# Kernel optimization log

Hardware: AMD Instinct MI355X
Metric: run time of the kernel (lower is better)

## Reference

```python
import jax, jax.numpy as jnp
import numpy as np

DIM = 512
HEADS = 4
HEAD_DIM = DIM // HEADS
HIDDEN = DIM * 2
DEPTH = 4
N = 32768
T = 4  # fixed branch/token dim


def _layernorm(x, w, b, eps=1e-5):
    m = jnp.mean(x, axis=-1, keepdims=True)
    v = jnp.mean(jnp.square(x - m), axis=-1, keepdims=True)
    return (x - m) * jax.lax.rsqrt(v + eps) * w + b


def setup_inputs() -> dict:
    key = jax.random.key(0)
    ks = jax.random.split(key, 24)
    s = 0.02
    d = {
        'x': jax.random.normal(ks[0], (N, DIM, T), dtype=jnp.float32),
        'branch_embed': s * jax.random.normal(ks[1], (T, DIM), dtype=jnp.float32),
        'ln1_w': jnp.ones((DEPTH, DIM), jnp.float32),
        'ln1_b': jnp.zeros((DEPTH, DIM), jnp.float32),
        'qkv_w': s * jax.random.normal(ks[2], (DEPTH, 3 * DIM, DIM), dtype=jnp.float32),
        'qkv_b': jnp.zeros((DEPTH, 3 * DIM), jnp.float32),
        'proj_w': s * jax.random.normal(ks[3], (DEPTH, DIM, DIM), dtype=jnp.float32),
        'proj_b': jnp.zeros((DEPTH, DIM), jnp.float32),
        'ln2_w': jnp.ones((DEPTH, DIM), jnp.float32),
        'ln2_b': jnp.zeros((DEPTH, DIM), jnp.float32),
        'ffn_w1': s * jax.random.normal(ks[4], (DEPTH, HIDDEN, DIM), dtype=jnp.float32),
        'ffn_b1': jnp.zeros((DEPTH, HIDDEN), jnp.float32),
        'ffn_w2': s * jax.random.normal(ks[5], (DEPTH, DIM, HIDDEN), dtype=jnp.float32),
        'ffn_b2': jnp.zeros((DEPTH, DIM), jnp.float32),
        'pool_q': s * jax.random.normal(ks[6], (DIM,), dtype=jnp.float32),
        'pool_w': s * jax.random.normal(ks[7], (DIM, DIM), dtype=jnp.float32),
        'out_ln_w': jnp.ones((DIM,), jnp.float32),
        'out_ln_b': jnp.zeros((DIM,), jnp.float32),
        'out_w1': s * jax.random.normal(ks[8], (DIM // 2, DIM), dtype=jnp.float32),
        'out_b1': jnp.zeros((DIM // 2,), jnp.float32),
        'out_w2': s * jax.random.normal(ks[9], (1, DIM // 2), dtype=jnp.float32),
        'out_b2': jnp.zeros((1,), jnp.float32),
    }
    return d


def reference(x, branch_embed, ln1_w, ln1_b, qkv_w, qkv_b, proj_w, proj_b,
              ln2_w, ln2_b, ffn_w1, ffn_b1, ffn_w2, ffn_b2,
              pool_q, pool_w, out_ln_w, out_ln_b, out_w1, out_b1, out_w2, out_b2):
    # (N, C, 4) -> (N, 4, C), add branch embedding
    x = jnp.swapaxes(x, 1, 2) + branch_embed[None]
    n = x.shape[0]
    scale = 1.0 / np.sqrt(HEAD_DIM)
    for i in range(DEPTH):
        # --- MHSA (pre-LN, eval mode -> dropout off) ---
        h = _layernorm(x, ln1_w[i], ln1_b[i])
        qkv = jnp.einsum('ntd,ed->nte', h, qkv_w[i]) + qkv_b[i]  # (N, T, 3D)
        q, k, v = jnp.split(qkv, 3, axis=-1)
        q = q.reshape(n, T, HEADS, HEAD_DIM).transpose(0, 2, 1, 3)
        k = k.reshape(n, T, HEADS, HEAD_DIM).transpose(0, 2, 1, 3)
        v = v.reshape(n, T, HEADS, HEAD_DIM).transpose(0, 2, 1, 3)
        scores = jnp.einsum('nhqd,nhkd->nhqk', q, k) * scale
        attn = jax.nn.softmax(scores, axis=-1)
        o = jnp.einsum('nhqk,nhkd->nhqd', attn, v)
        o = o.transpose(0, 2, 1, 3).reshape(n, T, DIM)
        o = jnp.einsum('ntd,ed->nte', o, proj_w[i]) + proj_b[i]
        x = x + o
        # --- FFN ---
        h = _layernorm(x, ln2_w[i], ln2_b[i])
        f = jax.nn.gelu(jnp.einsum('ntd,hd->nth', h, ffn_w1[i]) + ffn_b1[i], approximate=False)
        f = jnp.einsum('nth,dh->ntd', f, ffn_w2[i]) + ffn_b2[i]
        x = x + f
    # --- attention pooling head ---
    k = jnp.einsum('ntd,ed->nte', x, pool_w)            # pool_proj (no bias)
    score = jax.nn.softmax(jnp.einsum('d,ntd->nt', pool_q, k) / np.sqrt(DIM), axis=-1)
    z = jnp.einsum('nt,ntd->nd', score, x)
    z = _layernorm(z, out_ln_w, out_ln_b)
    z = jax.nn.gelu(z @ out_w1.T + out_b1, approximate=False)
    y = (z @ out_w2.T + out_b2)[:, 0]
    return y
```

## Files before the change

kernel.cpp:

```cpp
#include <hip/hip_runtime.h>

typedef unsigned short u16;
typedef unsigned int u32;
typedef __attribute__((ext_vector_type(8))) short s16x8;
typedef __attribute__((ext_vector_type(8))) unsigned short u16x8;
typedef __attribute__((ext_vector_type(4))) float f32x4;
typedef __attribute__((ext_vector_type(4))) unsigned int u32x4;

__device__ __forceinline__ u16 f2bf(float f) {
    u32 u = __float_as_uint(f);
    u32 r = (u + 0x7fffu + ((u >> 16) & 1u)) >> 16;
    return (u16)r;
}
__device__ __forceinline__ float bf2f(u16 u) { return __uint_as_float(((u32)u) << 16); }
__device__ __forceinline__ float bflo(u32 u) { return __uint_as_float(u << 16); }
__device__ __forceinline__ float bfhi(u32 u) { return __uint_as_float(u & 0xffff0000u); }
__device__ __forceinline__ float gelu_exact(float v) {
    return 0.5f * v * (1.0f + erff(v * 0.70710678118654752f));
}

__device__ __forceinline__ void gload16(const void* g, void* l) {
    __builtin_amdgcn_global_load_lds(
        (const __attribute__((address_space(1))) u32*)g,
        (__attribute__((address_space(3))) u32*)l, 16, 0, 0);
}

__global__ __launch_bounds__(256) void k_cvt5(const float* __restrict__ s0, u16* __restrict__ d0,
                                              const float* __restrict__ s1, u16* __restrict__ d1,
                                              const float* __restrict__ s2, u16* __restrict__ d2,
                                              const float* __restrict__ s3, u16* __restrict__ d3,
                                              const float* __restrict__ s4, u16* __restrict__ d4) {
    int i = blockIdx.x * 256 + threadIdx.x;
    const float* s; u16* d; int off;
    if (i < 786432)       { s = s0; d = d0; off = i; }
    else if (i < 1048576) { s = s1; d = d1; off = i - 786432; }
    else if (i < 1572864) { s = s2; d = d2; off = i - 1048576; }
    else if (i < 2097152) { s = s3; d = d3; off = i - 1572864; }
    else                  { s = s4; d = d4; off = i - 2097152; }
    float4 v = *(const float4*)(s + (size_t)off * 4);
    u16 o0 = f2bf(v.x), o1 = f2bf(v.y), o2 = f2bf(v.z), o3 = f2bf(v.w);
    uint2 o; o.x = (u32)o0 | ((u32)o1 << 16); o.y = (u32)o2 | ((u32)o3 << 16);
    *(uint2*)(d + (size_t)off * 4) = o;
}

__global__ __launch_bounds__(256) void k_poolq(const float* __restrict__ pq,
                                               const float* __restrict__ W,
                                               float* __restrict__ qw) {
    int d = blockIdx.x * 256 + threadIdx.x;
    float s = 0.f;
    for (int e = 0; e < 512; ++e) s += pq[e] * W[(size_t)e * 512 + d];
    qw[d] = s;
}

__global__ __launch_bounds__(256) void k_embed_ln(const float* __restrict__ x,
                                                  const float* __restrict__ be,
                                                  const float* __restrict__ w,
                                                  const float* __restrict__ b,
                                                  u16* __restrict__ Xb,
                                                  u16* __restrict__ Hb) {
    __shared__ u16 ld[4][512];
    int s = blockIdx.x;
    int tid = threadIdx.x;
    const float* xs = x + (size_t)s * 2048;
#pragma unroll
    for (int i = 0; i < 2; ++i) {
        int d = tid + i * 256;
        float4 v = *(const float4*)(xs + d * 4);
        ld[0][d] = f2bf(v.x + be[d]);
        ld[1][d] = f2bf(v.y + be[512 + d]);
        ld[2][d] = f2bf(v.z + be[1024 + d]);
        ld[3][d] = f2bf(v.w + be[1536 + d]);
    }
    __syncthreads();
    int t = tid >> 6, lane = tid & 63;
    u16x8 raw = *(const u16x8*)(&ld[t][lane * 8]);
    *(u16x8*)(Xb + ((size_t)s * 4 + t) * 512 + lane * 8) = raw;
    float a[8];
#pragma unroll
    for (int j = 0; j < 8; ++j) a[j] = bf2f(raw[j]);
    float s1 = 0.f, s2 = 0.f;
#pragma unroll
    for (int j = 0; j < 8; ++j) { s1 += a[j]; s2 += a[j] * a[j]; }
#pragma unroll
    for (int d = 1; d < 64; d <<= 1) { s1 += __shfl_xor(s1, d); s2 += __shfl_xor(s2, d); }
    float mean = s1 * (1.0f / 512.0f);
    float var  = s2 * (1.0f / 512.0f) - mean * mean;
    float rstd = rsqrtf(var + 1e-5f);
    float4 w0 = *(const float4*)(w + lane * 8);
    float4 w1 = *(const float4*)(w + lane * 8 + 4);
    float4 b0 = *(const float4*)(b + lane * 8);
    float4 b1 = *(const float4*)(b + lane * 8 + 4);
    float wv[8] = {w0.x, w0.y, w0.z, w0.w, w1.x, w1.y, w1.z, w1.w};
    float bv[8] = {b0.x, b0.y, b0.z, b0.w, b1.x, b1.y, b1.z, b1.w};
    u16x8 o;
#pragma unroll
    for (int j = 0; j < 8; ++j) o[j] = f2bf((a[j] - mean) * rstd * wv[j] + bv[j]);
    *(u16x8*)(Hb + ((size_t)s * 4 + t) * 512 + lane * 8) = o;
}

__global__ __launch_bounds__(256) void k_ln(const u16* __restrict__ Xb,
                                            const float* __restrict__ w,
                                            const float* __restrict__ b,
                                            u16* __restrict__ H) {
    int row = blockIdx.x * 4 + (threadIdx.x >> 6);
    int lane = threadIdx.x & 63;
    u16x8 xv = *(const u16x8*)(Xb + (size_t)row * 512 + lane * 8);
    float a[8];
#pragma unroll
    for (int j = 0; j < 8; ++j) a[j] = bf2f(xv[j]);
    float s1 = 0.f, s2 = 0.f;
#pragma unroll
    for (int j = 0; j < 8; ++j) { s1 += a[j]; s2 += a[j] * a[j]; }
#pragma unroll
    for (int d = 1; d < 64; d <<= 1) { s1 += __shfl_xor(s1, d); s2 += __shfl_xor(s2, d); }
    float mean = s1 * (1.0f / 512.0f);
    float var  = s2 * (1.0f / 512.0f) - mean * mean;
    float rstd = rsqrtf(var + 1e-5f);
    float4 w0 = *(const float4*)(w + lane * 8);
    float4 w1 = *(const float4*)(w + lane * 8 + 4);
    float4 b0 = *(const float4*)(b + lane * 8);
    float4 b1 = *(const float4*)(b + lane * 8 + 4);
    float wv[8] = {w0.x, w0.y, w0.z, w0.w, w1.x, w1.y, w1.z, w1.w};
    float bv[8] = {b0.x, b0.y, b0.z, b0.w, b1.x, b1.y, b1.z, b1.w};
    u16x8 o;
#pragma unroll
    for (int j = 0; j < 8; ++j) o[j] = f2bf((a[j] - mean) * rstd * wv[j] + bv[j]);
    *(u16x8*)(H + (size_t)row * 512 + lane * 8) = o;
}

template <bool BIAS, bool GELU_, bool RESID, bool BOUNCE, bool NT>
__global__ __launch_bounds__(512, 2) void k_gemm256(const u16* __restrict__ A,
                                                    const u16* __restrict__ W,
                                                    const float* __restrict__ bias,
                                                    u16* __restrict__ Cb,
                                                    u16* __restrict__ Xbres,
                                                    int K, int ncols, int TN, int T) {
    __shared__ __align__(16) u16 lds[2 * 32768];
    __shared__ __align__(16) u16 bounce[8192];
    int tid = threadIdx.x;
    int lane = tid & 63;
    int wid = tid >> 6;
    int G = gridDim.x, b = blockIdx.x;
    int start, end, step;
    if ((G & 7) == 0) {
        int xcd = b & 7, nxb = G >> 3, j = b >> 3;
        start = (int)(((long long)xcd * T) >> 3) + j;
        end   = (int)(((long long)(xcd + 1) * T) >> 3);
        step  = nxb;
    } else {
        start = (int)(((long long)b * T) / G);
        end   = (int)(((long long)(b + 1) * T) / G);
        step  = 1;
    }
    if (start >= end) return;
    int NS = K >> 6;
    int mgrp = wid >> 2, ngrp = wid & 3;

    f32x4 acc[8][4];
#pragma unroll
    for (int i = 0; i < 8; ++i)
#pragma unroll
        for (int j = 0; j < 4; ++j) acc[i][j] = (f32x4){0.f, 0.f, 0.f, 0.f};

    int srow = tid >> 3;
    int sel  = (((tid & 7) * 16) ^ ((srow & 7) << 4)) >> 1;
    size_t K64 = (size_t)K * 64;
    char* ldsB = (char*)lds;
    int wdst = wid * 1024;

    const u16 *cA0, *cA1, *cB0, *cB1, *nA0, *nA1, *nB0, *nB1;
    int cm0, cn0, nm0, nn0;
    auto tilePtrs = [&](int ti, const u16*& a0, const u16*& a1,
                        const u16*& b0, const u16*& b1, int& m0o, int& n0o) {
        int bx = ti / TN, by = ti - bx * TN;
        int m0 = bx * 256, n0 = by * 256;
        a0 = A + (size_t)(m0 + srow) * K + sel;
        a1 = A + (size_t)(m0 + 128 + srow) * K + sel;
        b0 = W + (size_t)(n0 + srow) * K + sel;
        b1 = W + (size_t)(n0 + 128 + srow) * K + sel;
        m0o = m0; n0o = n0;
    };

    auto S_Aq12 = [&](const u16* a0, const u16* a1, int s) {
        char* d = ldsB + (s & 1) * 65536 + wdst;
        gload16(a0 + (size_t)s * 64, d);
        gload16(a1 + (size_t)s * 64, d + 16384);
    };
    auto S_Aq34 = [&](const u16* a0, const u16* a1, int s) {
        char* d = ldsB + (s & 1) * 65536 + 8192 + wdst;
        gload16(a0 + K64 + (size_t)s * 64, d);
        gload16(a1 + K64 + (size_t)s * 64, d + 16384);
    };
    auto S_Blo = [&](const u16* b0, int s) {
        char* d = ldsB + (s & 1) * 65536 + 32768 + wdst;
        gload16(b0 + (size_t)s * 64, d);
        gload16(b0 + K64 + (size_t)s * 64, d + 8192);
    };
    auto S_Bhi = [&](const u16* b1, int s) {
        char* d = ldsB + (s & 1) * 65536 + 49152 + wdst;
        gload16(b1 + (size_t)s * 64, d);
        gload16(b1 + K64 + (size_t)s * 64, d + 8192);
    };

    int arow = mgrp * 128 + (lane & 15);
    int brow = ngrp * 64 + (lane & 15);
    int sub = (lane >> 4) << 4;
    int amask = ((arow & 7) << 4), bmask = ((brow & 7) << 4);
    int aoff0 = arow * 128 + (sub ^ amask);
    int boff0 = 32768 + brow * 128 + (sub ^ bmask);
    int aoff1 = arow * 128 + ((sub | 64) ^ amask);
    int boff1 = 32768 + brow * 128 + ((sub | 64) ^ bmask);

    tilePtrs(start, cA0, cA1, cB0, cB1, cm0, cn0);
    S_Blo(cB0, 0); S_Bhi(cB1, 0); S_Aq12(cA0, cA1, 0); S_Aq34(cA0, cA1, 0);
    S_Blo(cB0, 1); S_Bhi(cB1, 1); S_Aq12(cA0, cA1, 1);
    asm volatile("s_waitcnt vmcnt(6)" ::: "memory");
    __builtin_amdgcn_s_barrier();

    for (int ti = start; ti < end; ti += step) {
        bool hasNext = (ti + step < end);
        if (hasNext) tilePtrs(ti + step, nA0, nA1, nB0, nB1, nm0, nn0);

        s16x8 bfr[4][2];
        for (int s = 0; s < NS; ++s) {
            const char* sb = ldsB + (s & 1) * 65536;
            int st = s + 1, st2 = s + 2;
            bool n1 = st < NS, n2 = st2 < NS;
            s16x8 af[2][2];
#pragma unroll
            for (int ni = 0; ni < 4; ++ni) {
                bfr[ni][0] = *(const s16x8*)(sb + boff0 + ni * 2048);
                bfr[ni][1] = *(const s16x8*)(sb + boff1 + ni * 2048);
            }
            af[0][0] = *(const s16x8*)(sb + aoff0);
            af[0][1] = *(const s16x8*)(sb + aoff1);
            af[1][0] = *(const s16x8*)(sb + aoff0 + 2048);
            af[1][1] = *(const s16x8*)(sb + aoff1 + 2048);
            if (n1) S_Aq34(cA0, cA1, st); else if (hasNext) S_Aq34(nA0, nA1, st - NS);
            __builtin_amdgcn_s_barrier();
            __builtin_amdgcn_s_setprio(1);
#pragma unroll
            for (int mj = 0; mj < 2; ++mj)
#pragma unroll
                for (int ni = 0; ni < 4; ++ni) {
                    acc[mj][ni] = __builtin_amdgcn_mfma_f32_16x16x32_bf16(bfr[ni][0], af[mj][0], acc[mj][ni], 0, 0, 0);
                    acc[mj][ni] = __builtin_amdgcn_mfma_f32_16x16x32_bf16(bfr[ni][1], af[mj][1], acc[mj][ni], 0, 0, 0);
                }
            __builtin_amdgcn_s_setprio(0);
            __builtin_amdgcn_s_barrier();
#pragma unroll
            for (int mj = 0; mj < 2; ++mj) {
                af[mj][0] = *(const s16x8*)(sb + aoff0 + (2 + mj) * 2048);
                af[mj][1] = *(const s16x8*)(sb + aoff1 + (2 + mj) * 2048);
            }
            if (n2) S_Blo(cB0, st2); else if (hasNext) S_Blo(nB0, st2 - NS);
            __builtin_amdgcn_s_barrier();
            __builtin_amdgcn_s_setprio(1);
#pragma unroll
            for (int mj = 0; mj < 2; ++mj)
#pragma unroll
                for (int ni = 0; ni < 4; ++ni) {
                    acc[2 + mj][ni] = __builtin_amdgcn_mfma_f32_16x16x32_bf16(bfr[ni][0], af[mj][0], acc[2 + mj][ni], 0, 0, 0);
                    acc[2 + mj][ni] = __builtin_amdgcn_mfma_f32_16x16x32_bf16(bfr[ni][1], af[mj][1], acc[2 + mj][ni], 0, 0, 0);
                }
            __builtin_amdgcn_s_setprio(0);
            __builtin_amdgcn_s_barrier();
#pragma unroll
            for (int mj = 0; mj < 2; ++mj) {
                af[mj][0] = *(const s16x8*)(sb + aoff0 + (4 + mj) * 2048);
                af[mj][1] = *(const s16x8*)(sb + aoff1 + (4 + mj) * 2048);
            }
            if (n2) S_Bhi(cB1, st2); else if (hasNext) S_Bhi(nB1, st2 - NS);
            __builtin_amdgcn_s_barrier();
            __builtin_amdgcn_s_setprio(1);
#pragma unroll
            for (int mj = 0; mj < 2; ++mj)
#pragma unroll
                for (int ni = 0; ni < 4; ++ni) {
                    acc[4 + mj][ni] = __builtin_amdgcn_mfma_f32_16x16x32_bf16(bfr[ni][0], af[mj][0], acc[4 + mj][ni], 0, 0, 0);
                    acc[4 + mj][ni] = __builtin_amdgcn_mfma_f32_16x16x32_bf16(bfr[ni][1], af[mj][1], acc[4 + mj][ni], 0, 0, 0);
                }
            __builtin_amdgcn_s_setprio(0);
            __builtin_amdgcn_s_barrier();
#pragma unroll
            for (int mj = 0; mj < 2; ++mj) {
                af[mj][0] = *(const s16x8*)(sb + aoff0 + (6 + mj) * 2048);
                af[mj][1] = *(const s16x8*)(sb + aoff1 + (6 + mj) * 2048);
            }
            if (n2) S_Aq12(cA0, cA1, st2); else if (hasNext) S_Aq12(nA0, nA1, st2 - NS);
            __builtin_amdgcn_s_barrier();
            __builtin_amdgcn_s_setprio(1);
#pragma unroll
            for (int mj = 0; mj < 2; ++mj)
#pragma unroll
                for (int ni = 0; ni < 4; ++ni) {
                    acc[6 + mj][ni] = __builtin_amdgcn_mfma_f32_16x16x32_bf16(bfr[ni][0], af[mj][0], acc[6 + mj][ni], 0, 0, 0);
                    acc[6 + mj][ni] = __builtin_amdgcn_mfma_f32_16x16x32_bf16(bfr[ni][1], af[mj][1], acc[6 + mj][ni], 0, 0, 0);
                }
            __builtin_amdgcn_s_setprio(0);
            bool staged24 = n2 || hasNext;
            bool last = (s == NS - 1) && !hasNext;
            if (!last) {
                if (staged24) asm volatile("s_waitcnt vmcnt(6)" ::: "memory");
                else          asm volatile("s_waitcnt vmcnt(0)" ::: "memory");
                __builtin_amdgcn_s_barrier();
            }
        }

        int r_lane = lane & 15, cg = lane >> 4;
        float4 bb[4];
        if (BIAS) {
#pragma unroll
            for (int ni = 0; ni < 4; ++ni)
                bb[ni] = *(const float4*)(bias + cn0 + ngrp * 64 + ni * 16 + cg * 4);
        }
        if (BOUNCE) {
            u16* bw = bounce + wid * 1024;
            int qrow = lane >> 3, kc = lane & 7;
#pragma unroll
            for (int mi = 0; mi < 8; ++mi) {
                int rowbase = cm0 + mgrp * 128 + mi * 16;
#pragma unroll
                for (int ni = 0; ni < 4; ++ni) {
                    f32x4 v = acc[mi][ni];
                    if (BIAS) { v[0] += bb[ni].x; v[1] += bb[ni].y; v[2] += bb[ni].z; v[3] += bb[ni].w; }
                    if (GELU_) {
#pragma unroll
                        for (int j = 0; j < 4; ++j) v[j] = gelu_exact(v[j]);
                    }
                    uint2 o;
                    o.x = (u32)f2bf(v[0]) | ((u32)f2bf(v[1]) << 16);
                    o.y = (u32)f2bf(v[2]) | ((u32)f2bf(v[3]) << 16);
                    int slot = (4 * ni + cg) ^ (r_lane & 14);
                    *(uint2*)(bw + r_lane * 64 + slot * 4) = o;
                    acc[mi][ni] = (f32x4){0.f, 0.f, 0.f, 0.f};
                }
                asm volatile("s_waitcnt lgkmcnt(0)" ::: "memory");
#pragma unroll
                for (int h = 0; h < 2; ++h) {
                    int rd = h * 8 + qrow;
                    int e = (2 * kc) ^ (rd & 14);
                    u32x4 t = *(const u32x4*)(bw + rd * 64 + e * 4);
                    int row = rowbase + rd;
                    int c2 = cn0 + ngrp * 64 + kc * 8;
                    u16* dst = Cb + (size_t)row * ncols + c2;
                    if (NT) __builtin_nontemporal_store(t, (u32x4*)dst);
                    else    *(u32x4*)dst = t;
                }
                asm volatile("s_waitcnt lgkmcnt(0)" ::: "memory");
            }
        } else {
#pragma unroll
            for (int mi = 0; mi < 8; ++mi) {
                int row = cm0 + mgrp * 128 + mi * 16 + r_lane;
#pragma unroll
                for (int ni = 0; ni < 4; ++ni) {
                    int c = cn0 + ngrp * 64 + ni * 16 + cg * 4;
                    f32x4 v = acc[mi][ni];
                    if (BIAS) { v[0] += bb[ni].x; v[1] += bb[ni].y; v[2] += bb[ni].z; v[3] += bb[ni].w; }
                    if (GELU_) {
#pragma unroll
                        for (int j = 0; j < 4; ++j) v[j] = gelu_exact(v[j]);
                    }
                    if (RESID) {
                        u16* px = Xbres + (size_t)row * 512 + c;
                        uint2 xv = *(uint2*)px;
                        float x0 = bflo(xv.x) + v[0];
                        float x1 = bfhi(xv.x) + v[1];
                        float x2 = bflo(xv.y) + v[2];
                        float x3 = bfhi(xv.y) + v[3];
                        uint2 o;
                        o.x = (u32)f2bf(x0) | ((u32)f2bf(x1) << 16);
                        o.y = (u32)f2bf(x2) | ((u32)f2bf(x3) << 16);
                        *(uint2*)px = o;
                    } else {
                        u32 lo = (u32)f2bf(v[0]) | ((u32)f2bf(v[1]) << 16);
                        u32 hi = (u32)f2bf(v[2]) | ((u32)f2bf(v[3]) << 16);
                        uint2 o; o.x = lo; o.y = hi;
                        *(uint2*)(Cb + (size_t)row * ncols + c) = o;
                    }
                    acc[mi][ni] = (f32x4){0.f, 0.f, 0.f, 0.f};
                }
            }
        }
        cA0 = nA0; cA1 = nA1; cB0 = nB0; cB1 = nB1; cm0 = nm0; cn0 = nn0;
    }
}

__global__ __launch_bounds__(256) void k_attn(const u16* __restrict__ QKV, u16* __restrict__ O) {
    int task = blockIdx.x * 4 + (threadIdx.x >> 6);
    int lane = threadIdx.x & 63;
    int s = task >> 2, h = task & 3;
    const u16* base = QKV + (size_t)s * 4 * 1536 + h * 128;
    float q[4][2], k[4][2], v[4][2];
#pragma unroll
    for (int t = 0; t < 4; ++t) {
        const u16* row = base + t * 1536;
        u32 uq = *(const u32*)(row + lane * 2);
        u32 uk = *(const u32*)(row + 512 + lane * 2);
        u32 uv = *(const u32*)(row + 1024 + lane * 2);
        q[t][0] = bflo(uq); q[t][1] = bfhi(uq);
        k[t][0] = bflo(uk); k[t][1] = bfhi(uk);
        v[t][0] = bflo(uv); v[t][1] = bfhi(uv);
    }
    float sc[4][4];
#pragma unroll
    for (int i = 0; i < 4; ++i)
#pragma unroll
        for (int j = 0; j < 4; ++j) {
            float p = q[i][0] * k[j][0] + q[i][1] * k[j][1];
#pragma unroll
            for (int d = 1; d < 64; d <<= 1) p += __shfl_xor(p, d);
            sc[i][j] = p * 0.08838834764831845f;
        }
    float o[4][2];
#pragma unroll
    for (int i = 0; i < 4; ++i) {
        float mx = fmaxf(fmaxf(sc[i][0], sc[i][1]), fmaxf(sc[i][2], sc[i][3]));
        float e0 = expf(sc[i][0] - mx), e1 = expf(sc[i][1] - mx);
        float e2 = expf(sc[i][2] - mx), e3 = expf(sc[i][3] - mx);
        float inv = 1.0f / (e0 + e1 + e2 + e3);
        float a0 = e0 * inv, a1 = e1 * inv, a2 = e2 * inv, a3 = e3 * inv;
        o[i][0] = a0 * v[0][0] + a1 * v[1][0] + a2 * v[2][0] + a3 * v[3][0];
        o[i][1] = a0 * v[0][1] + a1 * v[1][1] + a2 * v[2][1] + a3 * v[3][1];
    }
#pragma unroll
    for (int i = 0; i < 4; ++i) {
        u32 pk = (u32)f2bf(o[i][0]) | ((u32)f2bf(o[i][1]) << 16);
        *(u32*)(O + ((size_t)s * 4 + i) * 512 + h * 128 + lane * 2) = pk;
    }
}

__global__ __launch_bounds__(256) void k_pool(const u16* __restrict__ Xb, const float* __restrict__ qw,
                                              const float* __restrict__ olnw, const float* __restrict__ olnb,
                                              u16* __restrict__ Zb) {
    int s = blockIdx.x * 4 + (threadIdx.x >> 6);
    int lane = threadIdx.x & 63;
    float4 q0 = *(const float4*)(qw + lane * 8);
    float4 q1 = *(const float4*)(qw + lane * 8 + 4);
    float qv[8] = {q0.x, q0.y, q0.z, q0.w, q1.x, q1.y, q1.z, q1.w};
    u16x8 xr[4];
    float dot[4];
#pragma unroll
    for (int t = 0; t < 4; ++t) {
        xr[t] = *(const u16x8*)(Xb + ((size_t)s * 4 + t) * 512 + lane * 8);
        float p = 0.f;
#pragma unroll
        for (int j = 0; j < 8; ++j) p += qv[j] * bf2f(xr[t][j]);
#pragma unroll
        for (int d = 1; d < 64; d <<= 1) p += __shfl_xor(p, d);
        dot[t] = p * 0.044194173824159216f;
    }
    float mx = fmaxf(fmaxf(dot[0], dot[1]), fmaxf(dot[2], dot[3]));
    float e[4], se = 0.f;
#pragma unroll
    for (int t = 0; t < 4; ++t) { e[t] = expf(dot[t] - mx); se += e[t]; }
    float inv = 1.0f / se;
    float z[8] = {0, 0, 0, 0, 0, 0, 0, 0};
#pragma unroll
    for (int t = 0; t < 4; ++t) {
        float scv = e[t] * inv;
#pragma unroll
        for (int j = 0; j < 8; ++j) z[j] += scv * bf2f(xr[t][j]);
    }
    float s1 = 0.f, s2 = 0.f;
#pragma unroll
    for (int j = 0; j < 8; ++j) { s1 += z[j]; s2 += z[j] * z[j]; }
#pragma unroll
    for (int d = 1; d < 64; d <<= 1) { s1 += __shfl_xor(s1, d); s2 += __shfl_xor(s2, d); }
    float mean = s1 * (1.0f / 512.0f);
    float var  = s2 * (1.0f / 512.0f) - mean * mean;
    float rstd = rsqrtf(var + 1e-5f);
    float4 w0 = *(const float4*)(olnw + lane * 8);
    float4 w1 = *(const float4*)(olnw + lane * 8 + 4);
    float4 b0 = *(const float4*)(olnb + lane * 8);
    float4 b1 = *(const float4*)(olnb + lane * 8 + 4);
    float wv[8] = {w0.x, w0.y, w0.z, w0.w, w1.x, w1.y, w1.z, w1.w};
    float bv[8] = {b0.x, b0.y, b0.z, b0.w, b1.x, b1.y, b1.z, b1.w};
    u16x8 o;
#pragma unroll
    for (int j = 0; j < 8; ++j) o[j] = f2bf((z[j] - mean) * rstd * wv[j] + bv[j]);
    *(u16x8*)(Zb + (size_t)s * 512 + lane * 8) = o;
}

__global__ __launch_bounds__(256) void k_out2(const u16* __restrict__ G, const float* __restrict__ w2,
                                              const float* __restrict__ b2, float* __restrict__ y) {
    int s = blockIdx.x * 4 + (threadIdx.x >> 6);
    int lane = threadIdx.x & 63;
    uint2 u = *(const uint2*)(G + (size_t)s * 256 + lane * 4);
    float4 wv = *(const float4*)(w2 + lane * 4);
    float p = bflo(u.x) * wv.x + bfhi(u.x) * wv.y + bflo(u.y) * wv.z + bfhi(u.y) * wv.w;
#pragma unroll
    for (int d = 1; d < 64; d <<= 1) p += __shfl_xor(p, d);
    if (lane == 0) y[s] = p + b2[0];
}

extern "C" void kernel_launch(void* const* d_in, const int* in_sizes, int n_in,
                              void* d_out, int out_size, void* d_ws, size_t ws_size,
                              hipStream_t stream) {
    const float* x     = (const float*)d_in[0];
    const float* be    = (const float*)d_in[1];
    const float* ln1w  = (const float*)d_in[2];
    const float* ln1b  = (const float*)d_in[3];
    const float* qkvw  = (const float*)d_in[4];
    const float* qkvb  = (const float*)d_in[5];
    const float* projw = (const float*)d_in[6];
    const float* projb = (const float*)d_in[7];
    const float* ln2w  = (const float*)d_in[8];
    const float* ln2b  = (const float*)d_in[9];
    const float* f1w   = (const float*)d_in[10];
    const float* f1b   = (const float*)d_in[11];
    const float* f2w   = (const float*)d_in[12];
    const float* f2b   = (const float*)d_in[13];
    const float* poolq = (const float*)d_in[14];
    const float* poolw = (const float*)d_in[15];
    const float* olnw  = (const float*)d_in[16];
    const float* olnb  = (const float*)d_in[17];
    const float* ow1   = (const float*)d_in[18];
    const float* ob1   = (const float*)d_in[19];
    const float* ow2   = (const float*)d_in[20];
    const float* ob2   = (const float*)d_in[21];
    float* y = (float*)d_out;

    int N = in_sizes[0] / 2048;

    char* p = (char*)d_ws;
    auto take = [&](size_t b) { char* r = p; p += (b + 255) & ~(size_t)255; return r; };
    u16* qkvWb  = (u16*)take((size_t)3145728 * 2);
    u16* projWb = (u16*)take((size_t)1048576 * 2);
    u16* f1Wb   = (u16*)take((size_t)2097152 * 2);
    u16* f2Wb   = (u16*)take((size_t)2097152 * 2);
    u16* ow1b   = (u16*)take((size_t)131072 * 2);
    float* qw   = (float*)take(512 * 4);
    size_t fixedB = (size_t)(p - (char*)d_ws);

    int S = N;
    while (S > 256 && fixedB + (size_t)S * 20480 + 65536 > ws_size) S >>= 1;
    int R = S * 4;
    int TM = R / 256;

    u16* Xb    = (u16*)take((size_t)R * 512 * 2);
    u16* Hb    = (u16*)take((size_t)R * 512 * 2);
    u16* QKVb  = (u16*)take((size_t)R * 1536 * 2);
    u16* Fb  = QKVb;
    u16* Gb  = (u16*)((char*)QKVb + (size_t)R * 512 * 2);
    u16* Zb  = Hb;

    k_cvt5<<<8320, 256, 0, stream>>>(qkvw, qkvWb, projw, projWb, f1w, f1Wb,
                                     f2w, f2Wb, ow1, ow1b);
    k_poolq<<<2, 256, 0, stream>>>(poolq, poolw, qw);

    auto gridFor = [](int T) { return T < 256 ? T : 256; };

    for (int c0 = 0; c0 < N; c0 += S) {
        const float* xin = x + (size_t)c0 * 2048;
        k_embed_ln<<<S, 256, 0, stream>>>(xin, be, ln1w, ln1b, Xb, Hb);
        for (int l = 0; l < 4; ++l) {
            if (l > 0)
                k_ln<<<R / 4, 256, 0, stream>>>(Xb, ln1w + l * 512, ln1b + l * 512, Hb);
            { int T = TM * 6;
              k_gemm256<true, false, false, true, true><<<gridFor(T), 512, 0, stream>>>(
                  Hb, qkvWb + (size_t)l * 786432, qkvb + l * 1536, QKVb, nullptr, 512, 1536, 6, T); }
            k_attn<<<S, 256, 0, stream>>>(QKVb, Hb);
            { int T = TM * 2;
              k_gemm256<true, false, true, false, false><<<gridFor(T), 512, 0, stream>>>(
                  Hb, projWb + (size_t)l * 262144, projb + l * 512, nullptr, Xb, 512, 512, 2, T); }
            k_ln<<<R / 4, 256, 0, stream>>>(Xb, ln2w + l * 512, ln2b + l * 512, Hb);
            { int T = TM * 4;
              k_gemm256<true, true, false, false, false><<<gridFor(T), 512, 0, stream>>>(
                  Hb, f1Wb + (size_t)l * 524288, f1b + l * 1024, Fb, nullptr, 512, 1024, 4, T); }
            { int T = TM * 2;
              k_gemm256<true, false, true, false, false><<<gridFor(T), 512, 0, stream>>>(
                  Fb, f2Wb + (size_t)l * 524288, f2b + l * 512, nullptr, Xb, 1024, 512, 2, T); }
        }
        k_pool<<<S / 4, 256, 0, stream>>>(Xb, qw, olnw, olnb, Zb);
        { int T = S / 256;
          k_gemm256<true, true, false, false, false><<<gridFor(T), 512, 0, stream>>>(
              Zb, ow1b, ob1, Gb, nullptr, 512, 256, 1, T); }
        k_out2<<<S / 4, 256, 0, stream>>>(Gb, ow2, ob2, y + c0);
    }
    (void)n_in; (void)out_size; (void)ws_size;
}
```

Measured before the change: 4.289 ms.

## Fold LayerNorm into GEMMs via precomputed row stats and weight column sums

Removes the standalone LayerNorm kernels. The LN gain is folded into the QKV and FFN1 weights at conversion time, and the epilogue applies rstd, mean times the weight column sum, and an adjusted bias. Row sum and sum-of-squares statistics are produced by the embed kernel and by atomics in the residual GEMM epilogues. Each stats buffer is zeroed inside the consuming GEMM. This saves a full read and write pass over the activations per LN, at the cost of atomics, ping-pong stats buffers, and a one-pass variance computation from bf16 values.

```diff
diff --git a/kernel.cpp b/kernel.cpp
--- a/kernel.cpp
+++ b/kernel.cpp
@@ -26,21 +26,60 @@
 }
 
 __global__ __launch_bounds__(256) void k_cvt5(const float* __restrict__ s0, u16* __restrict__ d0,
+                                              const float* __restrict__ g0,
                                               const float* __restrict__ s1, u16* __restrict__ d1,
                                               const float* __restrict__ s2, u16* __restrict__ d2,
+                                              const float* __restrict__ g2,
                                               const float* __restrict__ s3, u16* __restrict__ d3,
                                               const float* __restrict__ s4, u16* __restrict__ d4) {
     int i = blockIdx.x * 256 + threadIdx.x;
-    const float* s; u16* d; int off;
-    if (i < 786432)       { s = s0; d = d0; off = i; }
+    const float* s; u16* d; int off; const float* gm = nullptr; int gidx = 0;
+    if (i < 786432)       { s = s0; d = d0; off = i; gm = g0; gidx = (off / 196608) * 512 + (off & 127) * 4; }
     else if (i < 1048576) { s = s1; d = d1; off = i - 786432; }
-    else if (i < 1572864) { s = s2; d = d2; off = i - 1048576; }
+    else if (i < 1572864) { s = s2; d = d2; off = i - 1048576; gm = g2; gidx = (off / 131072) * 512 + (off & 127) * 4; }
     else if (i < 2097152) { s = s3; d = d3; off = i - 1572864; }
     else                  { s = s4; d = d4; off = i - 2097152; }
     float4 v = *(const float4*)(s + (size_t)off * 4);
+    if (gm) {
+        float4 g = *(const float4*)(gm + gidx);
+        v.x *= g.x; v.y *= g.y; v.z *= g.z; v.w *= g.w;
+    }
     u16 o0 = f2bf(v.x), o1 = f2bf(v.y), o2 = f2bf(v.z), o3 = f2bf(v.w);
     uint2 o; o.x = (u32)o0 | ((u32)o1 << 16); o.y = (u32)o2 | ((u32)o3 << 16);
     *(uint2*)(d + (size_t)off * 4) = o;
+}
+
+__global__ __launch_bounds__(256) void k_uv(const u16* __restrict__ Wq, const float* __restrict__ Wqf,
+                                            const float* __restrict__ bq, const float* __restrict__ betaq,
+                                            float* __restrict__ uq, float* __restrict__ b2q,
+                                            const u16* __restrict__ Wf, const float* __restrict__ Wff,
+                                            const float* __restrict__ bf_, const float* __restrict__ betaf,
+                                            float* __restrict__ uf, float* __restrict__ b2f) {
+    int wid = blockIdx.x * 4 + (threadIdx.x >> 6);
+    int lane = threadIdx.x & 63;
+    const u16* wrow; const float* frow; const float* beta; float bias0; float* up; float* b2p; int idx;
+    if (wid < 6144) {
+        int l = wid / 1536, c = wid - l * 1536;
+        size_t ro = ((size_t)l * 1536 + c) * 512;
+        wrow = Wq + ro; frow = Wqf + ro; beta = betaq + l * 512;
+        bias0 = bq[l * 1536 + c]; up = uq; b2p = b2q; idx = wid;
+    } else {
+        int w2 = wid - 6144;
+        int l = w2 / 1024, c = w2 - l * 1024;
+        size_t ro = ((size_t)l * 1024 + c) * 512;
+        wrow = Wf + ro; frow = Wff + ro; beta = betaf + l * 512;
+        bias0 = bf_[l * 1024 + c]; up = uf; b2p = b2f; idx = w2;
+    }
+    float su = 0.f, sb = 0.f;
+#pragma unroll
+    for (int j = 0; j < 8; ++j) {
+        int k = lane * 8 + j;
+        su += bf2f(wrow[k]);
+        sb += beta[k] * frow[k];
+    }
+#pragma unroll
+    for (int d = 1; d < 64; d <<= 1) { su += __shfl_xor(su, d); sb += __shfl_xor(sb, d); }
+    if (lane == 0) { up[idx] = su; b2p[idx] = bias0 + sb; }
 }
 
 __global__ __launch_bounds__(256) void k_poolq(const float* __restrict__ pq,
@@ -52,12 +91,10 @@
     qw[d] = s;
 }
 
-__global__ __launch_bounds__(256) void k_embed_ln(const float* __restrict__ x,
-                                                  const float* __restrict__ be,
-                                                  const float* __restrict__ w,
-                                                  const float* __restrict__ b,
-                                                  u16* __restrict__ Xb,
-                                                  u16* __restrict__ Hb) {
+__global__ __launch_bounds__(256) void k_embed(const float* __restrict__ x,
+                                               const float* __restrict__ be,
+                                               u16* __restrict__ Xb,
+                                               float2* __restrict__ S1) {
     __shared__ u16 ld[4][512];
     int s = blockIdx.x;
     int tid = threadIdx.x;
@@ -83,64 +120,30 @@
     for (int j = 0; j < 8; ++j) { s1 += a[j]; s2 += a[j] * a[j]; }
 #pragma unroll
     for (int d = 1; d < 64; d <<= 1) { s1 += __shfl_xor(s1, d); s2 += __shfl_xor(s2, d); }
-    float mean = s1 * (1.0f / 512.0f);
-    float var  = s2 * (1.0f / 512.0f) - mean * mean;
-    float rstd = rsqrtf(var + 1e-5f);
-    float4 w0 = *(const float4*)(w + lane * 8);
-    float4 w1 = *(const float4*)(w + lane * 8 + 4);
-    float4 b0 = *(const float4*)(b + lane * 8);
-    float4 b1 = *(const float4*)(b + lane * 8 + 4);
-    float wv[8] = {w0.x, w0.y, w0.z, w0.w, w1.x, w1.y, w1.z, w1.w};
-    float bv[8] = {b0.x, b0.y, b0.z, b0.w, b1.x, b1.y, b1.z, b1.w};
-    u16x8 o;
-#pragma unroll
-    for (int j = 0; j < 8; ++j) o[j] = f2bf((a[j] - mean) * rstd * wv[j] + bv[j]);
-    *(u16x8*)(Hb + ((size_t)s * 4 + t) * 512 + lane * 8) = o;
-}
-
-__global__ __launch_bounds__(256) void k_ln(const u16* __restrict__ Xb,
-                                            const float* __restrict__ w,
-                                            const float* __restrict__ b,
-                                            u16* __restrict__ H) {
-    int row = blockIdx.x * 4 + (threadIdx.x >> 6);
-    int lane = threadIdx.x & 63;
-    u16x8 xv = *(const u16x8*)(Xb + (size_t)row * 512 + lane * 8);
-    float a[8];
-#pragma unroll
-    for (int j = 0; j < 8; ++j) a[j] = bf2f(xv[j]);
-    float s1 = 0.f, s2 = 0.f;
-#pragma unroll
-    for (int j = 0; j < 8; ++j) { s1 += a[j]; s2 += a[j] * a[j]; }
-#pragma unroll
-    for (int d = 1; d < 64; d <<= 1) { s1 += __shfl_xor(s1, d); s2 += __shfl_xor(s2, d); }
-    float mean = s1 * (1.0f / 512.0f);
-    float var  = s2 * (1.0f / 512.0f) - mean * mean;
-    float rstd = rsqrtf(var + 1e-5f);
-    float4 w0 = *(const float4*)(w + lane * 8);
-    float4 w1 = *(const float4*)(w + lane * 8 + 4);
-    float4 b0 = *(const float4*)(b + lane * 8);
-    float4 b1 = *(const float4*)(b + lane * 8 + 4);
-    float wv[8] = {w0.x, w0.y, w0.z, w0.w, w1.x, w1.y, w1.z, w1.w};
-    float bv[8] = {b0.x, b0.y, b0.z, b0.w, b1.x, b1.y, b1.z, b1.w};
-    u16x8 o;
-#pragma unroll
-    for (int j = 0; j < 8; ++j) o[j] = f2bf((a[j] - mean) * rstd * wv[j] + bv[j]);
-    *(u16x8*)(H + (size_t)row * 512 + lane * 8) = o;
-}
-
-template <bool BIAS, bool GELU_, bool RESID, bool BOUNCE, bool NT>
+    if (lane == 0) S1[(size_t)s * 4 + t] = (float2){s1, s2};
+}
+
+template <bool BIAS, bool GELU_, bool RESID, bool BOUNCE, bool NT, bool LNIN, bool STATS>
 __global__ __launch_bounds__(512, 2) void k_gemm256(const u16* __restrict__ A,
                                                     const u16* __restrict__ W,
                                                     const float* __restrict__ bias,
                                                     u16* __restrict__ Cb,
                                                     u16* __restrict__ Xbres,
-                                                    int K, int ncols, int TN, int T) {
+                                                    const float2* __restrict__ Sin,
+                                                    float* __restrict__ Sout,
+                                                    const float* __restrict__ uvec,
+                                                    int K, int ncols, int TN, int T, int R) {
     __shared__ __align__(16) u16 lds[2 * 32768];
     __shared__ __align__(16) u16 bounce[8192];
     int tid = threadIdx.x;
     int lane = tid & 63;
     int wid = tid >> 6;
     int G = gridDim.x, b = blockIdx.x;
+    if (LNIN) {
+        float2* Sz = (float2*)Sout;
+        for (int i = b * 512 + tid; i < R; i += G * 512)
+            Sz[i] = (float2){0.f, 0.f};
+    }
     int start, end, step;
     if ((G & 7) == 0) {
         int xcd = b & 7, nxb = G >> 3, j = b >> 3;
@@ -314,6 +317,22 @@
             for (int ni = 0; ni < 4; ++ni)
                 bb[ni] = *(const float4*)(bias + cn0 + ngrp * 64 + ni * 16 + cg * 4);
         }
+        float4 uu[4];
+        float rho[8], mt[8];
+        if (LNIN) {
+#pragma unroll
+            for (int ni = 0; ni < 4; ++ni)
+                uu[ni] = *(const float4*)(uvec + cn0 + ngrp * 64 + ni * 16 + cg * 4);
+#pragma unroll
+            for (int mi = 0; mi < 8; ++mi) {
+                int row = cm0 + mgrp * 128 + mi * 16 + r_lane;
+                float2 sv = Sin[row];
+                float mu = sv.x * (1.0f / 512.0f);
+                float var = sv.y * (1.0f / 512.0f) - mu * mu;
+                float rr = rsqrtf(var + 1e-5f);
+                rho[mi] = rr; mt[mi] = mu * rr;
+            }
+        }
         if (BOUNCE) {
             u16* bw = bounce + wid * 1024;
             int qrow = lane >> 3, kc = lane & 7;
@@ -323,7 +342,14 @@
 #pragma unroll
                 for (int ni = 0; ni < 4; ++ni) {
                     f32x4 v = acc[mi][ni];
-                    if (BIAS) { v[0] += bb[ni].x; v[1] += bb[ni].y; v[2] += bb[ni].z; v[3] += bb[ni].w; }
+                    if (LNIN) {
+                        v[0] = rho[mi] * v[0] - mt[mi] * uu[ni].x + bb[ni].x;
+                        v[1] = rho[mi] * v[1] - mt[mi] * uu[ni].y + bb[ni].y;
+                        v[2] = rho[mi] * v[2] - mt[mi] * uu[ni].z + bb[ni].z;
+                        v[3] = rho[mi] * v[3] - mt[mi] * uu[ni].w + bb[ni].w;
+                    } else if (BIAS) {
+                        v[0] += bb[ni].x; v[1] += bb[ni].y; v[2] += bb[ni].z; v[3] += bb[ni].w;
+                    }
                     if (GELU_) {
 #pragma unroll
                         for (int j = 0; j < 4; ++j) v[j] = gelu_exact(v[j]);
@@ -353,11 +379,19 @@
 #pragma unroll
             for (int mi = 0; mi < 8; ++mi) {
                 int row = cm0 + mgrp * 128 + mi * 16 + r_lane;
+                float s1 = 0.f, s2 = 0.f;
 #pragma unroll
                 for (int ni = 0; ni < 4; ++ni) {
                     int c = cn0 + ngrp * 64 + ni * 16 + cg * 4;
                     f32x4 v = acc[mi][ni];
-                    if (BIAS) { v[0] += bb[ni].x; v[1] += bb[ni].y; v[2] += bb[ni].z; v[3] += bb[ni].w; }
+                    if (LNIN) {
+                        v[0] = rho[mi] * v[0] - mt[mi] * uu[ni].x + bb[ni].x;
+                        v[1] = rho[mi] * v[1] - mt[mi] * uu[ni].y + bb[ni].y;
+                        v[2] = rho[mi] * v[2] - mt[mi] * uu[ni].z + bb[ni].z;
+                        v[3] = rho[mi] * v[3] - mt[mi] * uu[ni].w + bb[ni].w;
+                    } else if (BIAS) {
+                        v[0] += bb[ni].x; v[1] += bb[ni].y; v[2] += bb[ni].z; v[3] += bb[ni].w;
+                    }
                     if (GELU_) {
 #pragma unroll
                         for (int j = 0; j < 4; ++j) v[j] = gelu_exact(v[j]);
@@ -373,6 +407,11 @@
                         o.x = (u32)f2bf(x0) | ((u32)f2bf(x1) << 16);
                         o.y = (u32)f2bf(x2) | ((u32)f2bf(x3) << 16);
                         *(uint2*)px = o;
+                        if (STATS) {
+                            float r0 = bflo(o.x), r1 = bfhi(o.x), r2 = bflo(o.y), r3 = bfhi(o.y);
+                            s1 += r0 + r1 + r2 + r3;
+                            s2 += r0 * r0 + r1 * r1 + r2 * r2 + r3 * r3;
+                        }
                     } else {
                         u32 lo = (u32)f2bf(v[0]) | ((u32)f2bf(v[1]) << 16);
                         u32 hi = (u32)f2bf(v[2]) | ((u32)f2bf(v[3]) << 16);
@@ -380,6 +419,14 @@
                         *(uint2*)(Cb + (size_t)row * ncols + c) = o;
                     }
                     acc[mi][ni] = (f32x4){0.f, 0.f, 0.f, 0.f};
+                }
+                if (STATS) {
+                    s1 += __shfl_xor(s1, 16); s2 += __shfl_xor(s2, 16);
+                    s1 += __shfl_xor(s1, 32); s2 += __shfl_xor(s2, 32);
+                    if (lane < 16) {
+                        atomicAdd(Sout + (size_t)row * 2, s1);
+                        atomicAdd(Sout + (size_t)row * 2 + 1, s2);
+                    }
                 }
             }
         }
@@ -532,51 +579,67 @@
     u16* f2Wb   = (u16*)take((size_t)2097152 * 2);
     u16* ow1b   = (u16*)take((size_t)131072 * 2);
     float* qw   = (float*)take(512 * 4);
+    float* u_qkv  = (float*)take(6144 * 4);
+    float* b2_qkv = (float*)take(6144 * 4);
+    float* u_f1   = (float*)take(4096 * 4);
+    float* b2_f1  = (float*)take(4096 * 4);
     size_t fixedB = (size_t)(p - (char*)d_ws);
 
     int S = N;
-    while (S > 256 && fixedB + (size_t)S * 20480 + 65536 > ws_size) S >>= 1;
+    while (S > 256 && fixedB + (size_t)S * 20544 + 65536 > ws_size) S >>= 1;
     int R = S * 4;
     int TM = R / 256;
 
     u16* Xb    = (u16*)take((size_t)R * 512 * 2);
     u16* Hb    = (u16*)take((size_t)R * 512 * 2);
     u16* QKVb  = (u16*)take((size_t)R * 1536 * 2);
+    float2* S1 = (float2*)take((size_t)R * 8);
+    float2* S2 = (float2*)take((size_t)R * 8);
     u16* Fb  = QKVb;
     u16* Gb  = (u16*)((char*)QKVb + (size_t)R * 512 * 2);
     u16* Zb  = Hb;
 
-    k_cvt5<<<8320, 256, 0, stream>>>(qkvw, qkvWb, projw, projWb, f1w, f1Wb,
-                                     f2w, f2Wb, ow1, ow1b);
+    k_cvt5<<<8320, 256, 0, stream>>>(qkvw, qkvWb, ln1w, projw, projWb,
+                                     f1w, f1Wb, ln2w, f2w, f2Wb, ow1, ow1b);
+    k_uv<<<2560, 256, 0, stream>>>(qkvWb, qkvw, qkvb, ln1b, u_qkv, b2_qkv,
+                                   f1Wb, f1w, f1b, ln2b, u_f1, b2_f1);
     k_poolq<<<2, 256, 0, stream>>>(poolq, poolw, qw);
 
     auto gridFor = [](int T) { return T < 256 ? T : 256; };
 
     for (int c0 = 0; c0 < N; c0 += S) {
         const float* xin = x + (size_t)c0 * 2048;
-        k_embed_ln<<<S, 256, 0, stream>>>(xin, be, ln1w, ln1b, Xb, Hb);
+        k_embed<<<S, 256, 0, stream>>>(xin, be, Xb, S1);
         for (int l = 0; l < 4; ++l) {
-            if (l > 0)
-                k_ln<<<R / 4, 256, 0, stream>>>(Xb, ln1w + l * 512, ln1b + l * 512, Hb);
             { int T = TM * 6;
-              k_gemm256<true, false, false, true, true><<<gridFor(T), 512, 0, stream>>>(
-                  Hb, qkvWb + (size_t)l * 786432, qkvb + l * 1536, QKVb, nullptr, 512, 1536, 6, T); }
+              k_gemm256<true, false, false, true, true, true, false><<<gridFor(T), 512, 0, stream>>>(
+                  Xb, qkvWb + (size_t)l * 786432, b2_qkv + l * 1536, QKVb, nullptr,
+                  S1, (float*)S2, u_qkv + l * 1536, 512, 1536, 6, T, R); }
             k_attn<<<S, 256, 0, stream>>>(QKVb, Hb);
             { int T = TM * 2;
-              k_gemm256<true, false, true, false, false><<<gridFor(T), 512, 0, stream>>>(
-                  Hb, projWb + (size_t)l * 262144, projb + l * 512, nullptr, Xb, 512, 512, 2, T); }
-            k_ln<<<R / 4, 256, 0, stream>>>(Xb, ln2w + l * 512, ln2b + l * 512, Hb);
+              k_gemm256<true, false, true, false, false, false, true><<<gridFor(T), 512, 0, stream>>>(
+                  Hb, projWb + (size_t)l * 262144, projb + l * 512, nullptr, Xb,
+                  nullptr, (float*)S2, nullptr, 512, 512, 2, T, R); }
             { int T = TM * 4;
-              k_gemm256<true, true, false, false, false><<<gridFor(T), 512, 0, stream>>>(
-                  Hb, f1Wb + (size_t)l * 524288, f1b + l * 1024, Fb, nullptr, 512, 1024, 4, T); }
-            { int T = TM * 2;
-              k_gemm256<true, false, true, false, false><<<gridFor(T), 512, 0, stream>>>(
-                  Fb, f2Wb + (size_t)l * 524288, f2b + l * 512, nullptr, Xb, 1024, 512, 2, T); }
+              k_gemm256<true, true, false, false, false, true, false><<<gridFor(T), 512, 0, stream>>>(
+                  Xb, f1Wb + (size_t)l * 524288, b2_f1 + l * 1024, Fb, nullptr,
+                  S2, (float*)S1, u_f1 + l * 1024, 512, 1024, 4, T, R); }
+            if (l < 3) {
+                int T = TM * 2;
+                k_gemm256<true, false, true, false, false, false, true><<<gridFor(T), 512, 0, stream>>>(
+                    Fb, f2Wb + (size_t)l * 524288, f2b + l * 512, nullptr, Xb,
+                    nullptr, (float*)S1, nullptr, 1024, 512, 2, T, R);
+            } else {
+                int T = TM * 2;
+                k_gemm256<true, false, true, false, false, false, false><<<gridFor(T), 512, 0, stream>>>(
+                    Fb, f2Wb + (size_t)l * 524288, f2b + l * 512, nullptr, Xb,
+                    nullptr, nullptr, nullptr, 1024, 512, 2, T, R);
+            }
         }
         k_pool<<<S / 4, 256, 0, stream>>>(Xb, qw, olnw, olnb, Zb);
         { int T = S / 256;
-          k_gemm256<true, true, false, false, false><<<gridFor(T), 512, 0, stream>>>(
-              Zb, ow1b, ob1, Gb, nullptr, 512, 256, 1, T); }
+          k_gemm256<true, true, false, false, false, false, false><<<gridFor(T), 512, 0, stream>>>(
+              Zb, ow1b, ob1, Gb, nullptr, nullptr, nullptr, nullptr, 512, 256, 1, T, R); }
         k_out2<<<S / 4, 256, 0, stream>>>(Gb, ow2, ob2, y + c0);
     }
     (void)n_in; (void)out_size; (void)ws_size;
```

Measured after the change: 3.949 ms (median of 2 runs). -7.9%, faster.
